# Kernel optimization log

Hardware: AMD Instinct MI355X
Metric: run time of the kernel (lower is better)

The kernel has to match this reference:

```python
import jax, jax.numpy as jnp
import numpy as np

IN_C, OUT_C, K, PAD = 64, 64, 3, 1
B, H, W = 8, 256, 256


def setup_inputs() -> dict:
    key = jax.random.key(0)
    k1, k2, k3, k4, k5 = jax.random.split(key, 5)
    x = jax.random.normal(k1, (B, IN_C, H, W), jnp.float32)
    # per-output-channel rank-1 CPD factors
    w1 = jax.random.normal(k2, (OUT_C, IN_C), jnp.float32) * 0.1   # 1x1 conv weights
    wh = jax.random.normal(k3, (OUT_C, K), jnp.float32) * 0.3      # 1xK horizontal kernels
    wv = jax.random.normal(k4, (OUT_C, K), jnp.float32) * 0.3      # Kx1 vertical kernels
    bias = jax.random.normal(k5, (OUT_C,), jnp.float32) * 0.01
    return {"x": x, "w1": w1, "wh": wh, "wv": wv, "bias": bias}


def _depthwise(y, w, kh, kw, ph, pw):
    # y: [B, C, H, W]; w: [C, kh*kw] -> depthwise conv with groups=C
    C = y.shape[1]
    kern = w.reshape(C, 1, kh, kw)
    return jax.lax.conv_general_dilated(
        y, kern, window_strides=(1, 1), padding=((ph, ph), (pw, pw)),
        dimension_numbers=("NCHW", "OIHW", "NCHW"), feature_group_count=C)


def reference(x, w1, wh, wv, bias):
    # Fused form of the per-branch loop: all branches share structure
    # 1x1 projection over in_channels -> one channel per branch
    y = jnp.einsum("bchw,oc->bohw", x, w1)          # [B, O, H, W]
    y = _depthwise(y, wh, 1, K, 0, PAD)              # 1xK horizontal conv
    y = _depthwise(y, wv, K, 1, PAD, 0)              # Kx1 vertical conv (bias last)
    return y + bias[None, :, None, None]
```

## Files before the change

kernel.cpp:

```cpp
#include <hip/hip_runtime.h>

#define NUM_B 8
#define NUM_C 64
#define NUM_O 64
#define DIM_H 256
#define DIM_W 256
#define SEG   4
#define TPB   512
#define XSS   72

typedef __attribute__((ext_vector_type(8))) short bf16x8;
typedef __attribute__((ext_vector_type(4))) float f32x4;

__device__ __forceinline__ unsigned bf16r(float f) {
    unsigned u = __float_as_uint(f);
    return (u + 0x7fffu + ((u >> 16) & 1u)) >> 16;
}
__device__ __forceinline__ unsigned cvt_pk_bf16(float lo, float hi) {
    unsigned r;
    asm("v_cvt_pk_bf16_f32 %0, %1, %2" : "=v"(r) : "v"(lo), "v"(hi));
    return r;
}

__global__ __launch_bounds__(TPB, 2)
void cpd_mfma(const float* __restrict__ x, const float* __restrict__ w1,
              const float* __restrict__ wh, const float* __restrict__ wv,
              const float* __restrict__ bias, float* __restrict__ out)
{
    __shared__ unsigned short xs[DIM_W + 2][XSS];

    const int tid  = threadIdx.x;
    const int lane = tid & 63;
    const int wave = tid >> 6;
    const int l15  = lane & 15;
    const int lhi  = lane >> 4;
    const int bx   = blockIdx.x;
    const int b    = bx >> 6;
    const int h0   = (bx & 63) * SEG;

    const int ot  = wave & 3;
    const int wh2 = wave >> 2;

    bf16x8 afrag[3][2];
    {
        const int o = ot * 16 + l15;
        const float a0 = wh[o*3+0], a1 = wh[o*3+1], a2 = wh[o*3+2];
        #pragma unroll
        for (int kb = 0; kb < 2; ++kb) {
            const float* wr = w1 + o * NUM_C + kb * 32 + lhi * 8;
            const float4 wa = *(const float4*)wr;
            const float4 wb = *(const float4*)(wr + 4);
            const float w8[8] = {wa.x,wa.y,wa.z,wa.w,wb.x,wb.y,wb.z,wb.w};
            #pragma unroll
            for (int i = 0; i < 8; ++i) {
                afrag[0][kb][i] = (short)bf16r(a0 * w8[i]);
                afrag[1][kb][i] = (short)bf16r(a1 * w8[i]);
                afrag[2][kb][i] = (short)bf16r(a2 * w8[i]);
            }
        }
    }
    float v0c[4], v1c[4], v2c[4], bc[4];
    #pragma unroll
    for (int r = 0; r < 4; ++r) {
        const int o = ot * 16 + lhi * 4 + r;
        v0c[r] = wv[o*3+0]; v1c[r] = wv[o*3+1]; v2c[r] = wv[o*3+2];
        bc[r]  = bias[o];
    }

    if (tid < XSS) { xs[0][tid] = 0; xs[DIM_W + 1][tid] = 0; }

    const int sw = tid & 255;
    const int ch = tid >> 8;
    const float* xb = x + (size_t)b * NUM_C * DIM_H * DIM_W + sw;

    float xr[32];
    if (h0 > 0) {
        #pragma unroll
        for (int p = 0; p < 8; ++p) {
            const int c0 = p * 8 + ch * 4;
            #pragma unroll
            for (int j = 0; j < 4; ++j)
                xr[p*4+j] = xb[(size_t)(c0+j) * (DIM_H*DIM_W) + (size_t)(h0-1) * DIM_W];
        }
    }

    f32x4 zP[8], zPP[8];
    #pragma unroll
    for (int t = 0; t < 8; ++t) {
        zP[t]  = (f32x4){0.f,0.f,0.f,0.f};
        zPP[t] = (f32x4){0.f,0.f,0.f,0.f};
    }

    __syncthreads();

    for (int hh = -1; hh <= SEG; ++hh) {
        const int h = h0 + hh;
        const bool hv = (h >= 0) && (h < DIM_H);

        __builtin_amdgcn_s_barrier();
        __builtin_amdgcn_sched_barrier(0);

        if (hv) {
            #pragma unroll
            for (int p = 0; p < 8; ++p) {
                const unsigned lo = cvt_pk_bf16(xr[p*4+0], xr[p*4+1]);
                const unsigned hi = cvt_pk_bf16(xr[p*4+2], xr[p*4+3]);
                *(uint2*)&xs[sw + 1][p * 8 + ch * 4] = make_uint2(lo, hi);
            }
        }
        if (hh < SEG && h + 1 < DIM_H) {
            #pragma unroll
            for (int p = 0; p < 8; ++p) {
                const int c0 = p * 8 + ch * 4;
                #pragma unroll
                for (int j = 0; j < 4; ++j)
                    xr[p*4+j] = xb[(size_t)(c0+j) * (DIM_H*DIM_W) + (size_t)(h+1) * DIM_W];
            }
        }

        asm volatile("s_waitcnt lgkmcnt(0)" ::: "memory");
        __builtin_amdgcn_s_barrier();
        __builtin_amdgcn_sched_barrier(0);

        f32x4 acc[8];
        #pragma unroll
        for (int t = 0; t < 8; ++t) acc[t] = (f32x4){0.f,0.f,0.f,0.f};

        if (hv) {
            const int cb = lhi * 8;
            #pragma unroll
            for (int t = 0; t < 8; ++t) {
                const unsigned short* rp0 = &xs[wh2 * 128 + t * 16 + l15][cb];
                #pragma unroll
                for (int s = 0; s < 3; ++s) {
                    const unsigned short* rp = rp0 + s * XSS;
                    const bf16x8 b0 = *(const bf16x8*)rp;
                    const bf16x8 b1 = *(const bf16x8*)(rp + 32);
                    acc[t] = __builtin_amdgcn_mfma_f32_16x16x32_bf16(afrag[s][0], b0, acc[t], 0, 0, 0);
                    acc[t] = __builtin_amdgcn_mfma_f32_16x16x32_bf16(afrag[s][1], b1, acc[t], 0, 0, 0);
                }
            }
        }

        if (hh >= 1) {
            float* ob = out + (size_t)b * NUM_O * DIM_H * DIM_W + (size_t)(h - 1) * DIM_W;
            #pragma unroll
            for (int t = 0; t < 8; ++t) {
                const int w = wh2 * 128 + t * 16 + l15;
                #pragma unroll
                for (int r = 0; r < 4; ++r) {
                    const int o = ot * 16 + lhi * 4 + r;
                    ob[(size_t)o * (DIM_H * DIM_W) + w] =
                        bc[r] + v0c[r]*zPP[t][r] + v1c[r]*zP[t][r] + v2c[r]*acc[t][r];
                }
            }
        }

        #pragma unroll
        for (int t = 0; t < 8; ++t) { zPP[t] = zP[t]; zP[t] = acc[t]; }
    }
}

extern "C" void kernel_launch(void* const* d_in, const int* in_sizes, int n_in,
                              void* d_out, int out_size, void* d_ws, size_t ws_size,
                              hipStream_t stream) {
    const float* x    = (const float*)d_in[0];
    const float* w1   = (const float*)d_in[1];
    const float* wh   = (const float*)d_in[2];
    const float* wv   = (const float*)d_in[3];
    const float* bias = (const float*)d_in[4];
    float* outp = (float*)d_out;
    cpd_mfma<<<dim3(NUM_B * (DIM_H / SEG)), dim3(TPB), 0, stream>>>(x, w1, wh, wv, bias, outp);
}
```

Before: 60.62 us.

## Split width into two halo tiles and double row segment per block

Each block now covers a 128-column width tile with one-column halos loaded from neighbouring columns, and processes 8 rows instead of 4. The grid size stays the same. Per-thread register use drops (fewer staged x values and accumulators), which allows launch bounds of 4 blocks per SM, and the vertical-conv weights move into shared memory. The aim is higher occupancy and proportionally less recomputation of the vertical-halo rows, at the cost of extra halo loads along width and fewer output columns per wave.

```diff
diff --git a/kernel.cpp b/kernel.cpp
--- a/kernel.cpp
+++ b/kernel.cpp
@@ -5,7 +5,8 @@
 #define NUM_O 64
 #define DIM_H 256
 #define DIM_W 256
-#define SEG   4
+#define SEG   8
+#define WT    128
 #define TPB   512
 #define XSS   72
 
@@ -22,12 +23,13 @@
     return r;
 }
 
-__global__ __launch_bounds__(TPB, 2)
+__global__ __launch_bounds__(TPB, 4)
 void cpd_mfma(const float* __restrict__ x, const float* __restrict__ w1,
               const float* __restrict__ wh, const float* __restrict__ wv,
               const float* __restrict__ bias, float* __restrict__ out)
 {
-    __shared__ unsigned short xs[DIM_W + 2][XSS];
+    __shared__ unsigned short xs[WT + 2][XSS];
+    __shared__ float wvb[NUM_O][4];
 
     const int tid  = threadIdx.x;
     const int lane = tid & 63;
@@ -35,11 +37,12 @@
     const int l15  = lane & 15;
     const int lhi  = lane >> 4;
     const int bx   = blockIdx.x;
+    const int w0   = (bx & 1) * WT;
+    const int h0   = ((bx >> 1) & 31) * SEG;
     const int b    = bx >> 6;
-    const int h0   = (bx & 63) * SEG;
 
-    const int ot  = wave & 3;
-    const int wh2 = wave >> 2;
+    const int ot = wave & 3;
+    const int wq = wave >> 2;
 
     bf16x8 afrag[3][2];
     {
@@ -59,42 +62,44 @@
             }
         }
     }
-    float v0c[4], v1c[4], v2c[4], bc[4];
-    #pragma unroll
-    for (int r = 0; r < 4; ++r) {
-        const int o = ot * 16 + lhi * 4 + r;
-        v0c[r] = wv[o*3+0]; v1c[r] = wv[o*3+1]; v2c[r] = wv[o*3+2];
-        bc[r]  = bias[o];
+
+    if (tid < NUM_O) {
+        wvb[tid][0] = wv[tid*3+0];
+        wvb[tid][1] = wv[tid*3+1];
+        wvb[tid][2] = wv[tid*3+2];
+        wvb[tid][3] = bias[tid];
+    }
+    if (tid < XSS) { xs[0][tid] = 0; xs[WT + 1][tid] = 0; }
+
+    const int sw = tid & (WT - 1);
+    const int ch = tid >> 7;
+    const float* xb = x + (size_t)b * NUM_C * DIM_H * DIM_W + w0 + sw;
+
+    const int  hc     = tid & 63;
+    const int  hside  = (tid >> 6) & 1;
+    const int  hwg    = w0 - 1 + hside * (WT + 1);
+    const bool hvalid = (tid < 128) && (hwg >= 0) && (hwg < DIM_W);
+    const float* hb   = x + ((size_t)(b * NUM_C + hc) * DIM_H) * DIM_W + hwg;
+
+    float xr[16];
+    float hx = 0.f;
+    if (h0 > 0) {
+        #pragma unroll
+        for (int q = 0; q < 4; ++q)
+            #pragma unroll
+            for (int j = 0; j < 4; ++j)
+                xr[q*4+j] = xb[(size_t)(ch*16+q*4+j)*(DIM_H*DIM_W) + (size_t)(h0-1)*DIM_W];
+        if (hvalid) hx = hb[(size_t)(h0-1)*DIM_W];
     }
 
-    if (tid < XSS) { xs[0][tid] = 0; xs[DIM_W + 1][tid] = 0; }
-
-    const int sw = tid & 255;
-    const int ch = tid >> 8;
-    const float* xb = x + (size_t)b * NUM_C * DIM_H * DIM_W + sw;
-
-    float xr[32];
-    if (h0 > 0) {
-        #pragma unroll
-        for (int p = 0; p < 8; ++p) {
-            const int c0 = p * 8 + ch * 4;
-            #pragma unroll
-            for (int j = 0; j < 4; ++j)
-                xr[p*4+j] = xb[(size_t)(c0+j) * (DIM_H*DIM_W) + (size_t)(h0-1) * DIM_W];
-        }
-    }
-
-    f32x4 zP[8], zPP[8];
+    f32x4 zP[4], zPP[4];
     #pragma unroll
-    for (int t = 0; t < 8; ++t) {
-        zP[t]  = (f32x4){0.f,0.f,0.f,0.f};
-        zPP[t] = (f32x4){0.f,0.f,0.f,0.f};
-    }
+    for (int t = 0; t < 4; ++t) { zP[t] = (f32x4){0,0,0,0}; zPP[t] = (f32x4){0,0,0,0}; }
 
     __syncthreads();
 
     for (int hh = -1; hh <= SEG; ++hh) {
-        const int h = h0 + hh;
+        const int  h  = h0 + hh;
         const bool hv = (h >= 0) && (h < DIM_H);
 
         __builtin_amdgcn_s_barrier();
@@ -102,62 +107,63 @@
 
         if (hv) {
             #pragma unroll
-            for (int p = 0; p < 8; ++p) {
-                const unsigned lo = cvt_pk_bf16(xr[p*4+0], xr[p*4+1]);
-                const unsigned hi = cvt_pk_bf16(xr[p*4+2], xr[p*4+3]);
-                *(uint2*)&xs[sw + 1][p * 8 + ch * 4] = make_uint2(lo, hi);
+            for (int q = 0; q < 4; ++q) {
+                const unsigned lo = cvt_pk_bf16(xr[q*4+0], xr[q*4+1]);
+                const unsigned hi = cvt_pk_bf16(xr[q*4+2], xr[q*4+3]);
+                *(uint2*)&xs[sw + 1][ch * 16 + q * 4] = make_uint2(lo, hi);
             }
+            if (tid < 128)
+                xs[hside * (WT + 1)][hc] = (unsigned short)(hvalid ? bf16r(hx) : 0u);
         }
         if (hh < SEG && h + 1 < DIM_H) {
             #pragma unroll
-            for (int p = 0; p < 8; ++p) {
-                const int c0 = p * 8 + ch * 4;
+            for (int q = 0; q < 4; ++q)
                 #pragma unroll
                 for (int j = 0; j < 4; ++j)
-                    xr[p*4+j] = xb[(size_t)(c0+j) * (DIM_H*DIM_W) + (size_t)(h+1) * DIM_W];
-            }
+                    xr[q*4+j] = xb[(size_t)(ch*16+q*4+j)*(DIM_H*DIM_W) + (size_t)(h+1)*DIM_W];
+            if (hvalid) hx = hb[(size_t)(h+1)*DIM_W];
         }
 
         asm volatile("s_waitcnt lgkmcnt(0)" ::: "memory");
         __builtin_amdgcn_s_barrier();
         __builtin_amdgcn_sched_barrier(0);
 
-        f32x4 acc[8];
+        f32x4 acc[4];
         #pragma unroll
-        for (int t = 0; t < 8; ++t) acc[t] = (f32x4){0.f,0.f,0.f,0.f};
+        for (int t = 0; t < 4; ++t) acc[t] = (f32x4){0.f,0.f,0.f,0.f};
 
         if (hv) {
             const int cb = lhi * 8;
             #pragma unroll
-            for (int t = 0; t < 8; ++t) {
-                const unsigned short* rp0 = &xs[wh2 * 128 + t * 16 + l15][cb];
+            for (int t = 0; t < 4; ++t) {
+                const unsigned short* rp0 = &xs[wq*64 + t*16 + l15][cb];
                 #pragma unroll
                 for (int s = 0; s < 3; ++s) {
                     const unsigned short* rp = rp0 + s * XSS;
                     const bf16x8 b0 = *(const bf16x8*)rp;
                     const bf16x8 b1 = *(const bf16x8*)(rp + 32);
-                    acc[t] = __builtin_amdgcn_mfma_f32_16x16x32_bf16(afrag[s][0], b0, acc[t], 0, 0, 0);
-                    acc[t] = __builtin_amdgcn_mfma_f32_16x16x32_bf16(afrag[s][1], b1, acc[t], 0, 0, 0);
+                    acc[t] = __builtin_amdgcn_mfma_f32_16x16x32_bf16(afrag[s][0], b0, acc[t], 0,0,0);
+                    acc[t] = __builtin_amdgcn_mfma_f32_16x16x32_bf16(afrag[s][1], b1, acc[t], 0,0,0);
                 }
             }
         }
 
         if (hh >= 1) {
-            float* ob = out + (size_t)b * NUM_O * DIM_H * DIM_W + (size_t)(h - 1) * DIM_W;
+            const int g = h - 1;
             #pragma unroll
-            for (int t = 0; t < 8; ++t) {
-                const int w = wh2 * 128 + t * 16 + l15;
+            for (int r = 0; r < 4; ++r) {
+                const int o = ot * 16 + lhi * 4 + r;
+                const float4 cf = *(const float4*)wvb[o];
+                float* ob = out + ((size_t)(b * NUM_O + o) * DIM_H + g) * DIM_W
+                                + w0 + wq * 64 + l15;
                 #pragma unroll
-                for (int r = 0; r < 4; ++r) {
-                    const int o = ot * 16 + lhi * 4 + r;
-                    ob[(size_t)o * (DIM_H * DIM_W) + w] =
-                        bc[r] + v0c[r]*zPP[t][r] + v1c[r]*zP[t][r] + v2c[r]*acc[t][r];
-                }
+                for (int t = 0; t < 4; ++t)
+                    ob[t * 16] = cf.w + cf.x * zPP[t][r] + cf.y * zP[t][r] + cf.z * acc[t][r];
             }
         }
 
         #pragma unroll
-        for (int t = 0; t < 8; ++t) { zPP[t] = zP[t]; zP[t] = acc[t]; }
+        for (int t = 0; t < 4; ++t) { zPP[t] = zP[t]; zP[t] = acc[t]; }
     }
 }
 
@@ -170,5 +176,5 @@
     const float* wv   = (const float*)d_in[3];
     const float* bias = (const float*)d_in[4];
     float* outp = (float*)d_out;
-    cpd_mfma<<<dim3(NUM_B * (DIM_H / SEG)), dim3(TPB), 0, stream>>>(x, w1, wh, wv, bias, outp);
+    cpd_mfma<<<dim3(NUM_B * 32 * 2), dim3(TPB), 0, stream>>>(x, w1, wh, wv, bias, outp);
 }
```

After: 59.86 us. About the same (-1.2%).
